# Performance work log

Hardware: AMD Instinct MI355X
Metric: run time of the kernel (lower is better)

Reference implementation:

```python
import jax, jax.numpy as jnp
import numpy as np

B, T, D, H = 2, 2048, 1024, 16
HD = D // H
SCALE = HD ** -0.5
NEG_INF = float(np.finfo(np.float32).min)


def setup_inputs() -> dict:
    key = jax.random.key(0)
    ks = jax.random.split(key, 10)
    s = 1.0 / np.sqrt(D)
    x = jax.random.normal(ks[0], (B, T, D), dtype=jnp.float32)
    # causal mask, True = keep, shape (B,1,T,T)
    mask = jnp.broadcast_to(jnp.tril(jnp.ones((T, T), dtype=bool)), (B, 1, T, T))
    Wq = jax.random.normal(ks[1], (D, D), dtype=jnp.float32) * s
    bq = jax.random.normal(ks[2], (D,), dtype=jnp.float32) * s
    Wk = jax.random.normal(ks[3], (D, D), dtype=jnp.float32) * s
    bk = jax.random.normal(ks[4], (D,), dtype=jnp.float32) * s
    Wv = jax.random.normal(ks[5], (D, D), dtype=jnp.float32) * s
    bv = jax.random.normal(ks[6], (D,), dtype=jnp.float32) * s
    Wo = jax.random.normal(ks[7], (D, D), dtype=jnp.float32) * s
    bo = jax.random.normal(ks[8], (D,), dtype=jnp.float32) * s
    return {"x": x, "mask": mask, "Wq": Wq, "bq": bq, "Wk": Wk, "bk": bk,
            "Wv": Wv, "bv": bv, "Wo": Wo, "bo": bo}


def _split_heads(t):
    # (B,T,D) -> (B,H,T,HD)
    return t.reshape(B, T, H, HD).transpose(0, 2, 1, 3)


def masked_rowwise_softmax(scores, mask):
    # mask: bool, True = keep; fully-masked rows return zeros.
    s = scores.astype(jnp.float32)
    masked = jnp.where(mask, s, NEG_INF)
    row_max = jnp.max(masked, axis=-1, keepdims=True)
    exps = jnp.exp(masked - row_max) * mask.astype(jnp.float32)
    denom = jnp.maximum(jnp.sum(exps, axis=-1, keepdims=True), 1e-12)
    return (exps / denom).astype(scores.dtype)


def reference(x, mask, Wq, bq, Wk, bk, Wv, bv, Wo, bo):
    q = _split_heads(x @ Wq.T + bq)
    k = _split_heads(x @ Wk.T + bk)
    v = _split_heads(x @ Wv.T + bv)
    scores = jnp.einsum('bhqd,bhkd->bhqk', q, k) * SCALE
    m = jnp.broadcast_to(mask, (B, H, T, T))
    attn = masked_rowwise_softmax(scores, m)
    y = jnp.einsum('bhqk,bhkd->bhqd', attn, v)
    y = y.transpose(0, 2, 1, 3).reshape(B, T, D)
    return y @ Wo.T + bo
```

## Files before the change

kernel.cpp:

```cpp
#include <hip/hip_runtime.h>

#define B_ 2
#define H_ 16
#define T_ 2048
#define D_ 1024
#define HD_ 64
#define NEG_HUGE (-3.402823466e38f)
#define QSCALE 0.18033688011112042f

typedef unsigned short u16;
typedef unsigned int u32;
typedef __attribute__((ext_vector_type(8))) short bf16x8;
typedef __attribute__((ext_vector_type(4))) float f32x4;

__device__ __forceinline__ u16 f2bf(float f) {
    u32 u = __builtin_bit_cast(u32, f);
    u += 0x7FFFu + ((u >> 16) & 1u);
    return (u16)(u >> 16);
}

__device__ __forceinline__ f32x4 mfma16(bf16x8 a, bf16x8 b, f32x4 c) {
    return __builtin_amdgcn_mfma_f32_16x16x32_bf16(a, b, c, 0, 0, 0);
}

__device__ __forceinline__ void gld16(const void* g, void* l) {
    __builtin_amdgcn_global_load_lds(
        (const __attribute__((address_space(1))) u32*)g,
        (__attribute__((address_space(3))) u32*)l, 16, 0, 0);
}

__global__ __launch_bounds__(256) void to_bf16(
    const float* __restrict__ x,  const float* __restrict__ wq,
    const float* __restrict__ wk, const float* __restrict__ wv,
    const float* __restrict__ wo, u16* __restrict__ dst)
{
    const size_t g = ((size_t)blockIdx.x * 256 + threadIdx.x) * 8;
    const float* src; size_t off;
    if      (g < (size_t)(4u << 20)) { src = x;  off = g; }
    else if (g < (size_t)(5u << 20)) { src = wq; off = g - (size_t)(4u << 20); }
    else if (g < (size_t)(6u << 20)) { src = wk; off = g - (size_t)(5u << 20); }
    else if (g < (size_t)(7u << 20)) { src = wv; off = g - (size_t)(6u << 20); }
    else                             { src = wo; off = g - (size_t)(7u << 20); }
    const float4 a = *(const float4*)&src[off];
    const float4 b = *(const float4*)&src[off + 4];
    ushort4 lo = make_ushort4(f2bf(a.x), f2bf(a.y), f2bf(a.z), f2bf(a.w));
    ushort4 hi = make_ushort4(f2bf(b.x), f2bf(b.y), f2bf(b.z), f2bf(b.w));
    *(ushort4*)&dst[g]     = lo;
    *(ushort4*)&dst[g + 4] = hi;
}

__device__ __forceinline__ void gemm128_core(
    const u16* __restrict__ P0, const u16* __restrict__ P1,
    const int m0, const int n0, u16* As, u16* Bs, f32x4 (&acc)[4][4])
{
    const int tid  = threadIdx.x;
    const int lane = tid & 63;
    const int quad = lane >> 4;
    const int l15  = lane & 15;
    const int w    = tid >> 6;
    const int wm   = (w >> 1) << 6;
    const int wn   = (w & 1) << 6;
    const int swz  = l15 & 7;

    size_t aoff[4], boff[4];
    int    loff[4];
#pragma unroll
    for (int i = 0; i < 4; ++i) {
        const int slot = i * 256 + tid;
        const int r = slot >> 3, c = slot & 7;
        const int gc = ((c ^ (r & 7)) << 3);
        aoff[i] = (size_t)(m0 + r) * D_ + gc;
        boff[i] = (size_t)(n0 + r) * D_ + gc;
        loff[i] = slot * 8;
    }
    int rowA[4], rowB[4];
#pragma unroll
    for (int i = 0; i < 4; ++i) {
        rowA[i] = (wm + i * 16 + l15) * 64;
        rowB[i] = (wn + i * 16 + l15) * 64;
    }

    for (int k0 = 0; k0 < D_; k0 += 64) {
        __syncthreads();
#pragma unroll
        for (int i = 0; i < 4; ++i) {
            gld16(&P0[aoff[i] + k0], &As[loff[i]]);
            gld16(&P1[boff[i] + k0], &Bs[loff[i]]);
        }
        __syncthreads();
#pragma unroll
        for (int s = 0; s < 2; ++s) {
            const int ch = (((s << 2) + quad) ^ swz) << 3;
            bf16x8 af[4], bf[4];
#pragma unroll
            for (int mi = 0; mi < 4; ++mi) af[mi] = *(const bf16x8*)&As[rowA[mi] + ch];
#pragma unroll
            for (int ni = 0; ni < 4; ++ni) bf[ni] = *(const bf16x8*)&Bs[rowB[ni] + ch];
#pragma unroll
            for (int mi = 0; mi < 4; ++mi)
#pragma unroll
                for (int ni = 0; ni < 4; ++ni)
                    acc[mi][ni] = mfma16(af[mi], bf[ni], acc[mi][ni]);
        }
    }
}

__global__ __launch_bounds__(256) void gemm_qkv(
    const u16* __restrict__ xb,
    const u16* __restrict__ Wqb, const u16* __restrict__ Wkb, const u16* __restrict__ Wvb,
    const float* __restrict__ bq, const float* __restrict__ bk, const float* __restrict__ bv,
    u16* __restrict__ Qb, u16* __restrict__ Kb, u16* __restrict__ Vtb)
{
    __shared__ u16 As[128 * 64];
    __shared__ u16 Bs[128 * 64];
    const int z = blockIdx.z;

    f32x4 acc[4][4];
#pragma unroll
    for (int i = 0; i < 4; ++i)
#pragma unroll
        for (int j = 0; j < 4; ++j) acc[i][j] = (f32x4){0.f, 0.f, 0.f, 0.f};

    const int tid  = threadIdx.x;
    const int lane = tid & 63;
    const int quad = lane >> 4;
    const int l15  = lane & 15;
    const int w    = tid >> 6;
    const int wm   = (w >> 1) << 6;
    const int wn   = (w & 1) << 6;

    if (z < 2) {
        const u16*   W    = z ? Wkb : Wqb;
        const float* bias = z ? bk  : bq;
        const float  CF   = z ? 1.f : QSCALE;
        u16*         C    = z ? Kb  : Qb;
        const int m0 = blockIdx.x << 7;
        const int n0 = blockIdx.y << 7;
        gemm128_core(W, xb, m0, n0, As, Bs, acc);

        const int fbase = m0 + wm;
        const int hbase = fbase >> 6;
        const int tbase = n0 + wn;
#pragma unroll
        for (int i = 0; i < 4; ++i) {
            const int hd0 = i * 16 + (quad << 2);
            const float4 bi = *(const float4*)&bias[fbase + hd0];
#pragma unroll
            for (int j = 0; j < 4; ++j) {
                const int tg = tbase + j * 16 + l15;
                const int b = tg >> 11, t = tg & 2047;
                f32x4 a = acc[i][j];
                ushort4 v = make_ushort4(f2bf((a[0] + bi.x) * CF),
                                         f2bf((a[1] + bi.y) * CF),
                                         f2bf((a[2] + bi.z) * CF),
                                         f2bf((a[3] + bi.w) * CF));
                *(ushort4*)&C[((size_t)((b << 4) + hbase) * T_ + t) * HD_ + hd0] = v;
            }
        }
    } else {
        const int m0 = blockIdx.y << 7;
        const int n0 = blockIdx.x << 7;
        gemm128_core(xb, Wvb, m0, n0, As, Bs, acc);

        u16* scr = ((w < 2) ? As : Bs) + ((w & 1) ? 4096 : 0);
        __syncthreads();

        const int pq   = quad >> 1;
        const int psub = (quad & 1) << 2;
#pragma unroll
        for (int j = 0; j < 4; ++j) {
            const int row = j * 16 + l15;
            const float bi = bv[n0 + wn + row];
            const int sw = row & 7;
#pragma unroll
            for (int i = 0; i < 4; ++i) {
                f32x4 a = acc[i][j];
                ushort4 v = make_ushort4(f2bf(a[0] + bi), f2bf(a[1] + bi),
                                         f2bf(a[2] + bi), f2bf(a[3] + bi));
                *(ushort4*)&scr[row * 64 + (((2 * i + pq) ^ sw) << 3) + psub] = v;
            }
        }
        __asm__ volatile("s_waitcnt lgkmcnt(0)" ::: "memory");

        const int b  = (m0 + wm) >> 11;
        const int t0 = (m0 + wm) & 2047;
        const int h  = (n0 + wn) >> 6;
#pragma unroll
        for (int e = 0; e < 8; ++e) {
            const int hdl = (lane >> 3) + e * 8;
            const int c   = lane & 7;
            bf16x8 vv = *(const bf16x8*)&scr[hdl * 64 + ((c ^ (hdl & 7)) << 3)];
            *(bf16x8*)&Vtb[((size_t)((b << 4) + h) * HD_ + hdl) * T_ + t0 + (c << 3)] = vv;
        }
    }
}

__global__ __launch_bounds__(256) void gemm_out(
    const u16* __restrict__ Ab, const u16* __restrict__ Wob,
    const float* __restrict__ bo, float* __restrict__ C)
{
    __shared__ u16 As[128 * 64];
    __shared__ u16 Bs[128 * 64];
    const int m0 = blockIdx.y << 7;
    const int n0 = blockIdx.x << 7;

    f32x4 acc[4][4];
#pragma unroll
    for (int i = 0; i < 4; ++i)
#pragma unroll
        for (int j = 0; j < 4; ++j) acc[i][j] = (f32x4){0.f, 0.f, 0.f, 0.f};

    gemm128_core(Ab, Wob, m0, n0, As, Bs, acc);

    const int tid  = threadIdx.x;
    const int lane = tid & 63;
    const int quad = lane >> 4;
    const int l15  = lane & 15;
    const int w    = tid >> 6;
    const int wm   = (w >> 1) << 6;
    const int wn   = (w & 1) << 6;

    float bi[4];
#pragma unroll
    for (int ni = 0; ni < 4; ++ni) bi[ni] = bo[n0 + wn + ni * 16 + l15];

#pragma unroll
    for (int mi = 0; mi < 4; ++mi) {
        const int m = m0 + wm + mi * 16 + (quad << 2);
#pragma unroll
        for (int r = 0; r < 4; ++r)
#pragma unroll
            for (int ni = 0; ni < 4; ++ni)
                C[(size_t)(m + r) * D_ + n0 + wn + ni * 16 + l15] = acc[mi][ni][r] + bi[ni];
    }
}

__global__ __launch_bounds__(256) void attn_mfma(
    const u16* __restrict__ Qg, const u16* __restrict__ Kg,
    const u16* __restrict__ Vtg, u16* __restrict__ Out)
{
    __shared__ u16 Ks[128 * 64];
    __shared__ u16 Vs[64 * 128];
    __shared__ u16 Ps[4 * 16 * 128];
    const int tid  = threadIdx.x;
    const int w    = tid >> 6;
    const int lane = tid & 63;
    const int quad = lane >> 4;
    const int l15  = lane & 15;
    const int bh   = blockIdx.x;
    const int qt   = (T_ / 64 - 1) - blockIdx.y;
    const size_t base = (size_t)bh * (T_ * HD_);

    const int qloc = (w << 4) + l15;
    const int qrow = (qt << 6) + qloc;
    const bf16x8 qf0 = *(const bf16x8*)&Qg[base + (size_t)qrow * HD_ + quad * 8];
    const bf16x8 qf1 = *(const bf16x8*)&Qg[base + (size_t)qrow * HD_ + 32 + quad * 8];

    f32x4 o[4];
#pragma unroll
    for (int nt = 0; nt < 4; ++nt) o[nt] = (f32x4){0.f, 0.f, 0.f, 0.f};
    float m_i = NEG_HUGE, l_i = 0.f;

    int lK[4], lV[4];
    size_t gK[4], gV[4];
#pragma unroll
    for (int i = 0; i < 4; ++i) {
        const int slot = i * 256 + tid;
        const int rk = slot >> 3, ck = slot & 7;
        lK[i] = rk * 64 + ((ck ^ (rk & 7)) << 3);
        gK[i] = base + (size_t)rk * HD_ + ck * 8;
        const int rv = slot >> 4, cv = slot & 15;
        lV[i] = rv * 128 + ((cv ^ (rv & 15)) << 3);
        gV[i] = base + (size_t)rv * T_ + cv * 8;
    }

    const int nIter = (qt + 2) >> 1;
    bf16x8 kreg[4], vreg[4];
#pragma unroll
    for (int i = 0; i < 4; ++i) {
        kreg[i] = *(const bf16x8*)&Kg[gK[i]];
        vreg[i] = *(const bf16x8*)&Vtg[gV[i]];
    }

    u16* Pw = &Ps[w * 16 * 128];
    const int swz7 = l15 & 7;

    for (int it = 0; it < nIter; ++it) {
        __syncthreads();
#pragma unroll
        for (int i = 0; i < 4; ++i) {
            *(bf16x8*)&Ks[lK[i]] = kreg[i];
            *(bf16x8*)&Vs[lV[i]] = vreg[i];
        }
        if (it + 1 < nIter) {
            const int koff = (it + 1) << 7;
#pragma unroll
            for (int i = 0; i < 4; ++i) {
                kreg[i] = *(const bf16x8*)&Kg[gK[i] + (size_t)koff * HD_];
                vreg[i] = *(const bf16x8*)&Vtg[gV[i] + koff];
            }
        }
        __syncthreads();

        f32x4 st[8];
#pragma unroll
        for (int t = 0; t < 8; ++t) {
            const int kr = (t * 16 + l15) * 64;
            const bf16x8 k0 = *(const bf16x8*)&Ks[kr + ((quad ^ swz7) << 3)];
            const bf16x8 k1 = *(const bf16x8*)&Ks[kr + (((quad + 4) ^ swz7) << 3)];
            f32x4 a = (f32x4){0.f, 0.f, 0.f, 0.f};
            a = mfma16(k0, qf0, a);
            a = mfma16(k1, qf1, a);
            st[t] = a;
        }

        if (it == nIter - 1) {
            const int koff = it << 7;
#pragma unroll
            for (int t = 0; t < 8; ++t)
#pragma unroll
                for (int r = 0; r < 4; ++r) {
                    const int kg = koff + t * 16 + (quad << 2) + r;
                    if (kg > qrow) st[t][r] = NEG_HUGE;
                }
        }

        float mx = st[0][0];
#pragma unroll
        for (int t = 0; t < 8; ++t)
#pragma unroll
            for (int r = 0; r < 4; ++r) mx = fmaxf(mx, st[t][r]);
        mx = fmaxf(mx, __shfl_xor(mx, 16, 64));
        mx = fmaxf(mx, __shfl_xor(mx, 32, 64));
        const float newm  = fmaxf(m_i, mx);
        const float alpha = exp2f(m_i - newm);
        float rs = 0.f;
#pragma unroll
        for (int t = 0; t < 8; ++t)
#pragma unroll
            for (int r = 0; r < 4; ++r) {
                const float e = exp2f(st[t][r] - newm);
                st[t][r] = e;
                rs += e;
            }
        rs += __shfl_xor(rs, 16, 64);
        rs += __shfl_xor(rs, 32, 64);
        l_i = l_i * alpha + rs;
        m_i = newm;

        const int pq   = quad >> 1;
        const int psub = (quad & 1) << 2;
#pragma unroll
        for (int t = 0; t < 8; ++t)
            *(ushort4*)&Pw[l15 * 128 + (((2 * t + pq) ^ l15) << 3) + psub] =
                make_ushort4(f2bf(st[t][0]), f2bf(st[t][1]),
                             f2bf(st[t][2]), f2bf(st[t][3]));
        __asm__ volatile("s_waitcnt lgkmcnt(0)" ::: "memory");

        float ar[4];
#pragma unroll
        for (int r = 0; r < 4; ++r) ar[r] = __shfl(alpha, (quad << 2) + r, 64);

        bf16x8 pf[4];
#pragma unroll
        for (int kq = 0; kq < 4; ++kq)
            pf[kq] = *(const bf16x8*)&Pw[l15 * 128 + ((((kq << 2) + quad) ^ l15) << 3)];

#pragma unroll
        for (int nt = 0; nt < 4; ++nt) {
            f32x4 oo = o[nt];
            oo[0] *= ar[0]; oo[1] *= ar[1]; oo[2] *= ar[2]; oo[3] *= ar[3];
            const int vr = (nt * 16 + l15) * 128;
#pragma unroll
            for (int kq = 0; kq < 4; ++kq) {
                const bf16x8 vf = *(const bf16x8*)&Vs[vr + ((((kq << 2) + quad) ^ l15) << 3)];
                oo = mfma16(pf[kq], vf, oo);
            }
            o[nt] = oo;
        }
    }

    float lr[4];
#pragma unroll
    for (int r = 0; r < 4; ++r)
        lr[r] = 1.f / fmaxf(__shfl(l_i, (quad << 2) + r, 64), 1e-12f);

    const int b = bh >> 4, h = bh & 15;
#pragma unroll
    for (int nt = 0; nt < 4; ++nt)
#pragma unroll
        for (int r = 0; r < 4; ++r) {
            const int qg2 = (qt << 6) + (w << 4) + (quad << 2) + r;
            Out[(size_t)(b * T_ + qg2) * D_ + (h << 6) + nt * 16 + l15] =
                f2bf(o[nt][r] * lr[r]);
        }
}

extern "C" void kernel_launch(void* const* d_in, const int* in_sizes, int n_in,
                              void* d_out, int out_size, void* d_ws, size_t ws_size,
                              hipStream_t stream)
{
    const float* x  = (const float*)d_in[0];
    const float* Wq = (const float*)d_in[2];
    const float* bq = (const float*)d_in[3];
    const float* Wk = (const float*)d_in[4];
    const float* bk = (const float*)d_in[5];
    const float* Wv = (const float*)d_in[6];
    const float* bv = (const float*)d_in[7];
    const float* Wo = (const float*)d_in[8];
    const float* bo = (const float*)d_in[9];
    float* out = (float*)d_out;

    const size_t M1 = (size_t)1 << 20;
    u16* wsu = (u16*)d_ws;
    u16* xb  = wsu;
    u16* wqb = wsu + 4 * M1;
    u16* wkb = wsu + 5 * M1;
    u16* wvb = wsu + 6 * M1;
    u16* wob = wsu + 7 * M1;
    u16* Qb  = wsu + 8 * M1;
    u16* Kb  = wsu + 12 * M1;
    u16* Vtb = wsu + 16 * M1;
    u16* AOb = wsu + 20 * M1;

    to_bf16<<<4096, 256, 0, stream>>>(x, Wq, Wk, Wv, Wo, wsu);

    dim3 gq(D_ / 128, (B_ * T_) / 128, 3);
    gemm_qkv<<<gq, 256, 0, stream>>>(xb, wqb, wkb, wvb, bq, bk, bv, Qb, Kb, Vtb);

    dim3 ga(B_ * H_, T_ / 64);
    attn_mfma<<<ga, 256, 0, stream>>>(Qb, Kb, Vtb, AOb);

    dim3 go(D_ / 128, (B_ * T_) / 128);
    gemm_out<<<go, 256, 0, stream>>>(AOb, wob, bo, out);
}
```

Baseline: 228.0 us.

## Stage Q/K epilogue through LDS, reuse K tile for P, cheaper bf16 pack

The Q/K projection epilogue now writes results into a swizzled LDS scratch and then emits coalesced 16-byte rows to global memory, replacing scattered 8-byte stores. The attention kernel drops its separate P buffer and writes P into the K shared tile after an added barrier, which shrinks LDS use and may raise occupancy. Float-to-bf16 conversion switches from round-to-nearest-even to round-half-up with a byte-permute pack. The change adds barriers and slightly alters rounding.

```diff
diff --git a/kernel.cpp b/kernel.cpp
--- a/kernel.cpp
+++ b/kernel.cpp
@@ -17,6 +17,19 @@
     u32 u = __builtin_bit_cast(u32, f);
     u += 0x7FFFu + ((u >> 16) & 1u);
     return (u16)(u >> 16);
+}
+
+__device__ __forceinline__ u32 pk2bf(float f0, float f1) {
+    const u32 a0 = __builtin_bit_cast(u32, f0) + 0x8000u;
+    const u32 a1 = __builtin_bit_cast(u32, f1) + 0x8000u;
+    return __builtin_amdgcn_perm(a1, a0, 0x07060302u);
+}
+
+__device__ __forceinline__ uint2 pk4bf(f32x4 a) {
+    uint2 r;
+    r.x = pk2bf(a[0], a[1]);
+    r.y = pk2bf(a[2], a[3]);
+    return r;
 }
 
 __device__ __forceinline__ f32x4 mfma16(bf16x8 a, bf16x8 b, f32x4 c) {
@@ -128,6 +141,10 @@
     const int w    = tid >> 6;
     const int wm   = (w >> 1) << 6;
     const int wn   = (w & 1) << 6;
+    const int pq   = quad >> 1;
+    const int psub = (quad & 1) << 2;
+
+    u16* scr = ((w < 2) ? As : Bs) + ((w & 1) ? 4096 : 0);
 
     if (z < 2) {
         const u16*   W    = z ? Wkb : Wqb;
@@ -137,36 +154,40 @@
         const int m0 = blockIdx.x << 7;
         const int n0 = blockIdx.y << 7;
         gemm128_core(W, xb, m0, n0, As, Bs, acc);
-
-        const int fbase = m0 + wm;
-        const int hbase = fbase >> 6;
-        const int tbase = n0 + wn;
+        __syncthreads();
+
+        const int fb = m0 + wm;
+        const int h  = fb >> 6;
+        const int tb = n0 + wn;
 #pragma unroll
         for (int i = 0; i < 4; ++i) {
-            const int hd0 = i * 16 + (quad << 2);
-            const float4 bi = *(const float4*)&bias[fbase + hd0];
+            const float4 bi = *(const float4*)&bias[fb + i * 16 + (quad << 2)];
 #pragma unroll
             for (int j = 0; j < 4; ++j) {
-                const int tg = tbase + j * 16 + l15;
-                const int b = tg >> 11, t = tg & 2047;
+                const int tl = j * 16 + l15;
                 f32x4 a = acc[i][j];
-                ushort4 v = make_ushort4(f2bf((a[0] + bi.x) * CF),
-                                         f2bf((a[1] + bi.y) * CF),
-                                         f2bf((a[2] + bi.z) * CF),
-                                         f2bf((a[3] + bi.w) * CF));
-                *(ushort4*)&C[((size_t)((b << 4) + hbase) * T_ + t) * HD_ + hd0] = v;
+                f32x4 v = { (a[0] + bi.x) * CF, (a[1] + bi.y) * CF,
+                            (a[2] + bi.z) * CF, (a[3] + bi.w) * CF };
+                *(uint2*)&scr[tl * 64 + (((2 * i + pq) ^ (tl & 7)) << 3) + psub] = pk4bf(v);
             }
+        }
+        __asm__ volatile("s_waitcnt lgkmcnt(0)" ::: "memory");
+
+        const int b  = tb >> 11;
+        const int t0 = tb & 2047;
+#pragma unroll
+        for (int e = 0; e < 8; ++e) {
+            const int tl = (lane >> 3) + e * 8;
+            const int c  = lane & 7;
+            bf16x8 v = *(const bf16x8*)&scr[tl * 64 + ((c ^ (tl & 7)) << 3)];
+            *(bf16x8*)&C[((size_t)((b << 4) + h) * T_ + t0 + tl) * HD_ + (c << 3)] = v;
         }
     } else {
         const int m0 = blockIdx.y << 7;
         const int n0 = blockIdx.x << 7;
         gemm128_core(xb, Wvb, m0, n0, As, Bs, acc);
-
-        u16* scr = ((w < 2) ? As : Bs) + ((w & 1) ? 4096 : 0);
-        __syncthreads();
-
-        const int pq   = quad >> 1;
-        const int psub = (quad & 1) << 2;
+        __syncthreads();
+
 #pragma unroll
         for (int j = 0; j < 4; ++j) {
             const int row = j * 16 + l15;
@@ -175,9 +196,8 @@
 #pragma unroll
             for (int i = 0; i < 4; ++i) {
                 f32x4 a = acc[i][j];
-                ushort4 v = make_ushort4(f2bf(a[0] + bi), f2bf(a[1] + bi),
-                                         f2bf(a[2] + bi), f2bf(a[3] + bi));
-                *(ushort4*)&scr[row * 64 + (((2 * i + pq) ^ sw) << 3) + psub] = v;
+                f32x4 v = { a[0] + bi, a[1] + bi, a[2] + bi, a[3] + bi };
+                *(uint2*)&scr[row * 64 + (((2 * i + pq) ^ sw) << 3) + psub] = pk4bf(v);
             }
         }
         __asm__ volatile("s_waitcnt lgkmcnt(0)" ::: "memory");
@@ -241,7 +261,6 @@
 {
     __shared__ u16 Ks[128 * 64];
     __shared__ u16 Vs[64 * 128];
-    __shared__ u16 Ps[4 * 16 * 128];
     const int tid  = threadIdx.x;
     const int w    = tid >> 6;
     const int lane = tid & 63;
@@ -282,8 +301,10 @@
         vreg[i] = *(const bf16x8*)&Vtg[gV[i]];
     }
 
-    u16* Pw = &Ps[w * 16 * 128];
+    u16* Pw = &Ks[w * 2048];
     const int swz7 = l15 & 7;
+    const int pq   = quad >> 1;
+    const int psub = (quad & 1) << 2;
 
     for (int it = 0; it < nIter; ++it) {
         __syncthreads();
@@ -348,13 +369,11 @@
         l_i = l_i * alpha + rs;
         m_i = newm;
 
-        const int pq   = quad >> 1;
-        const int psub = (quad & 1) << 2;
+        __syncthreads();
+
 #pragma unroll
         for (int t = 0; t < 8; ++t)
-            *(ushort4*)&Pw[l15 * 128 + (((2 * t + pq) ^ l15) << 3) + psub] =
-                make_ushort4(f2bf(st[t][0]), f2bf(st[t][1]),
-                             f2bf(st[t][2]), f2bf(st[t][3]));
+            *(uint2*)&Pw[l15 * 128 + (((2 * t + pq) ^ l15) << 3) + psub] = pk4bf(st[t]);
         __asm__ volatile("s_waitcnt lgkmcnt(0)" ::: "memory");
 
         float ar[4];
@@ -391,8 +410,8 @@
 #pragma unroll
         for (int r = 0; r < 4; ++r) {
             const int qg2 = (qt << 6) + (w << 4) + (quad << 2) + r;
-            Out[(size_t)(b * T_ + qg2) * D_ + (h << 6) + nt * 16 + l15] =
-                f2bf(o[nt][r] * lr[r]);
+            const u32 u = __builtin_bit_cast(u32, o[nt][r] * lr[r]) + 0x8000u;
+            Out[(size_t)(b * T_ + qg2) * D_ + (h << 6) + nt * 16 + l15] = (u16)(u >> 16);
         }
 }
 
```

Measured after the change: 226.2 us. No clear change (-0.8%).
